# Performance work log

Hardware: AMD Instinct MI355X
Metric: run time of the kernel (lower is better)

Reference implementation:

```python
import jax, jax.numpy as jnp
import numpy as np
from jax import lax

PEAK_THRESH = 0.1
PAF_SCORE_THRESH = 0.05
PAF_COUNT_THRESH = 0.8
P = 30   # max peaks kept per joint (vectorized stand-in for data-dependent nonzero())
S = 10   # samples along each limb line (torch.linspace steps=10)

# standard COCO person skeleton: 19 limbs over 17 keypoints
SKELETON = np.array([
    [15, 13], [13, 11], [16, 14], [14, 12], [11, 12], [5, 11], [6, 12], [5, 6],
    [5, 7], [6, 8], [7, 9], [8, 10], [1, 2], [0, 1], [0, 2], [1, 3], [2, 4],
    [3, 5], [4, 6],
])  # (L=19, 2)


def setup_inputs() -> dict:
    key = jax.random.key(0)
    k1, k2 = jax.random.split(key)
    heat_pred = jax.random.uniform(k1, (32, 17, 160, 160), dtype=jnp.float32)
    paf_pred = jax.random.normal(k2, (32, 38, 160, 160), dtype=jnp.float32)
    return {"heat_pred": heat_pred, "paf_pred": paf_pred}


def _forward(heat_pred, paf_pred):
    B, K, H, W = heat_pred.shape
    L = SKELETON.shape[0]

    # ---- 3x3 peak NMS (max_pool2d k=3, s=1, p=1) ----
    pooled = lax.reduce_window(heat_pred, -jnp.inf, lax.max,
                               (1, 1, 3, 3), (1, 1, 1, 1), 'SAME')
    is_peak = (heat_pred == pooled) & (heat_pred > PEAK_THRESH)

    # ---- dense subpixel (1D Newton) offsets ----
    r = jnp.roll(heat_pred, -1, -1); l = jnp.roll(heat_pred, 1, -1)
    d = jnp.roll(heat_pred, -1, -2); u = jnp.roll(heat_pred, 1, -2)
    dx_raw = 0.5 * (r - l); dy_raw = 0.5 * (d - u)
    dxx = r + l - 2.0 * heat_pred; dyy = d + u - 2.0 * heat_pred
    safe_dxx = jnp.where(jnp.abs(dxx) > 1e-6, -dxx, 1.0)
    safe_dyy = jnp.where(jnp.abs(dyy) > 1e-6, -dyy, 1.0)
    dx = jnp.where(jnp.abs(dxx) > 1e-6, dx_raw / safe_dxx, dx_raw)
    dy = jnp.where(jnp.abs(dyy) > 1e-6, dy_raw / safe_dyy, dy_raw)
    xi = jnp.arange(W); yi = jnp.arange(H)
    interior = (((yi > 0) & (yi < H - 1))[:, None]
                & ((xi > 0) & (xi < W - 1))[None, :])
    dx = jnp.where(interior, dx, 0.0)
    dy = jnp.where(interior, dy, 0.0)

    # ---- top-P peaks per (batch, joint) ----
    NEG = jnp.float32(-1e9)
    flat = jnp.where(is_peak, heat_pred, NEG).reshape(B, K, H * W)
    scores, idx = lax.top_k(flat, P)                    # (B, K, P)
    valid = scores > PEAK_THRESH
    py = (idx // W).astype(jnp.float32)
    px = (idx % W).astype(jnp.float32)
    dxp = jnp.take_along_axis(dx.reshape(B, K, H * W), idx, axis=2)
    dyp = jnp.take_along_axis(dy.reshape(B, K, H * W), idx, axis=2)
    px = jnp.where(valid, px + dxp, 0.0)
    py = jnp.where(valid, py + dyp, 0.0)
    sc = jnp.where(valid, scores, 0.0)
    peaks = jnp.stack([px, py, sc], axis=-1)            # (B, K, P, 3)

    # ---- PAF line-integral connection scores for all candidate pairs ----
    a = SKELETON[:, 0]; b = SKELETON[:, 1]
    ax, ay, sa, va = px[:, a], py[:, a], sc[:, a], valid[:, a]   # (B, L, P)
    bx, by, sb, vb = px[:, b], py[:, b], sc[:, b], valid[:, b]
    dxl = bx[:, :, None, :] - ax[:, :, :, None]          # (B, L, P, P)
    dyl = by[:, :, None, :] - ay[:, :, :, None]
    norm = jnp.sqrt(dxl * dxl + dyl * dyl) + 1e-8
    vx = dxl / norm; vy = dyl / norm
    t = jnp.linspace(0.0, 1.0, S, dtype=jnp.float32)     # (S,)
    xs = ax[:, :, :, None, None] + t * dxl[..., None]    # (B, L, P, P, S)
    ys = ay[:, :, :, None, None] + t * dyl[..., None]
    ix = jnp.clip(jnp.round(xs), 0, W - 1).astype(jnp.int32)
    iy = jnp.clip(jnp.round(ys), 0, H - 1).astype(jnp.int32)
    lin = (iy * W + ix).reshape(B, L, P * P * S)
    paf = paf_pred.reshape(B, L, 2, H * W)
    vals_x = jnp.take_along_axis(paf[:, :, 0], lin, axis=2).reshape(B, L, P, P, S)
    vals_y = jnp.take_along_axis(paf[:, :, 1], lin, axis=2).reshape(B, L, P, P, S)
    vecs = vals_x * vx[..., None] + vals_y * vy[..., None]
    mean_score = vecs.mean(-1)                            # (B, L, P, P)
    valid_ratio = (vecs > PAF_SCORE_THRESH).astype(jnp.float32).mean(-1)
    pair_valid = va[:, :, :, None] & vb[:, :, None, :]
    cond = (mean_score > 0.0) & (valid_ratio > PAF_COUNT_THRESH) & pair_valid
    conn = jnp.where(cond,
                     mean_score + 0.5 * (sa[:, :, :, None] + sb[:, :, None, :]),
                     0.0)                                 # (B, L, P, P)
    return peaks, conn


def reference(heat_pred, paf_pred):
    return _forward(heat_pred, paf_pred)
```

## Files before the change

### kernel.cpp

```cpp
#include <hip/hip_runtime.h>
#include <cstdint>
#include <cstddef>
#include <cfloat>

static constexpr int BATCH = 32;
static constexpr int KJ    = 17;
static constexpr int LL    = 19;
static constexpr int HH    = 160;
static constexpr int WW    = 160;
static constexpr int PPK   = 30;
static constexpr int SS    = 10;
static constexpr int HW    = HH * WW;
static constexpr int CAP   = 4096;
static constexpr int CELLS = HW / 4;
static constexpr int CGW   = WW / 4;

__constant__ int d_ska[LL] = {15,13,16,14,11,5,6,5,5,6,7,8,1,0,0,1,2,3,4};
__constant__ int d_skb[LL] = {13,11,14,12,12,11,12,6,7,8,9,10,2,1,2,3,4,5,6};
__constant__ float d_ts[SS] = {
    0.0f,
    (float)(1.0/9.0), (float)(2.0/9.0), (float)(3.0/9.0),
    (float)(4.0/9.0), (float)(5.0/9.0), (float)(6.0/9.0),
    (float)(7.0/9.0), (float)(8.0/9.0),
    1.0f
};

__device__ __forceinline__ float max3f(float a, float b, float c) {
    return fmaxf(fmaxf(a, b), c);
}
__device__ __forceinline__ unsigned long long umax64(unsigned long long a, unsigned long long b) {
    return a > b ? a : b;
}

__global__ __launch_bounds__(256, 4) void peaks_kernel(const float* __restrict__ heat,
                                                       float* __restrict__ out)
{
    const int ch = blockIdx.x;
    const float* hp = heat + (size_t)ch * HW;

    __shared__ unsigned long long keys[CAP];
    __shared__ unsigned long long sel4[4 * PPK];
    __shared__ unsigned long long sel[PPK];
    __shared__ int cnt;

    const int tid  = threadIdx.x;
    const int lane = tid & 63;
    const int wave = tid >> 6;
    const unsigned long long ltmask = ((unsigned long long)1 << lane) - 1ull;

    if (tid == 0) cnt = 0;
    __syncthreads();

    for (int c = tid; c < CELLS; c += 256) {
        int y  = c / CGW;
        int cg = c - y * CGW;
        int x0 = cg * 4;
        int yu = (y > 0) ? y - 1 : 0;
        int yd = (y < HH - 1) ? y + 1 : HH - 1;

        const float* rc = hp + y  * WW + x0;
        const float* ru = hp + yu * WW + x0;
        const float* rd = hp + yd * WW + x0;

        float4 vc = *(const float4*)rc;
        float4 vu = *(const float4*)ru;
        float4 vd = *(const float4*)rd;
        bool hasL = (x0 > 0);
        bool hasR = (x0 + 4 < WW);
        float lc = hasL ? rc[-1] : -FLT_MAX;
        float lu = hasL ? ru[-1] : -FLT_MAX;
        float ld = hasL ? rd[-1] : -FLT_MAX;
        float rcx = hasR ? rc[4] : -FLT_MAX;
        float rux = hasR ? ru[4] : -FLT_MAX;
        float rdx = hasR ? rd[4] : -FLT_MAX;

        float mu0 = max3f(lu, vu.x, vu.y), mu1 = max3f(vu.x, vu.y, vu.z);
        float mu2 = max3f(vu.y, vu.z, vu.w), mu3 = max3f(vu.z, vu.w, rux);
        float mc0 = max3f(lc, vc.x, vc.y), mc1 = max3f(vc.x, vc.y, vc.z);
        float mc2 = max3f(vc.y, vc.z, vc.w), mc3 = max3f(vc.z, vc.w, rcx);
        float md0 = max3f(ld, vd.x, vd.y), md1 = max3f(vd.x, vd.y, vd.z);
        float md2 = max3f(vd.y, vd.z, vd.w), md3 = max3f(vd.z, vd.w, rdx);

        float nm0 = max3f(mu0, mc0, md0);
        float nm1 = max3f(mu1, mc1, md1);
        float nm2 = max3f(mu2, mc2, md2);
        float nm3 = max3f(mu3, mc3, md3);

        bool pk0 = (vc.x == nm0) && (vc.x > 0.1f);
        bool pk1 = (vc.y == nm1) && (vc.y > 0.1f);
        bool pk2 = (vc.z == nm2) && (vc.z > 0.1f);
        bool pk3 = (vc.w == nm3) && (vc.w > 0.1f);

        unsigned long long b0 = __ballot(pk0);
        unsigned long long b1 = __ballot(pk1);
        unsigned long long b2 = __ballot(pk2);
        unsigned long long b3 = __ballot(pk3);
        int c0 = __popcll(b0), c1 = __popcll(b1), c2 = __popcll(b2), c3 = __popcll(b3);
        int tot = c0 + c1 + c2 + c3;
        int base = 0;
        if (lane == 0 && tot > 0) base = atomicAdd(&cnt, tot);
        base = __shfl(base, 0);

        int idx0 = y * WW + x0;
        if (pk0) {
            int slot = base + __popcll(b0 & ltmask);
            if (slot < CAP)
                keys[slot] = ((unsigned long long)__float_as_uint(vc.x) << 32)
                           | (unsigned long long)(0xFFFFFFFFu - (unsigned)(idx0 + 0));
        }
        if (pk1) {
            int slot = base + c0 + __popcll(b1 & ltmask);
            if (slot < CAP)
                keys[slot] = ((unsigned long long)__float_as_uint(vc.y) << 32)
                           | (unsigned long long)(0xFFFFFFFFu - (unsigned)(idx0 + 1));
        }
        if (pk2) {
            int slot = base + c0 + c1 + __popcll(b2 & ltmask);
            if (slot < CAP)
                keys[slot] = ((unsigned long long)__float_as_uint(vc.z) << 32)
                           | (unsigned long long)(0xFFFFFFFFu - (unsigned)(idx0 + 2));
        }
        if (pk3) {
            int slot = base + c0 + c1 + c2 + __popcll(b3 & ltmask);
            if (slot < CAP)
                keys[slot] = ((unsigned long long)__float_as_uint(vc.w) << 32)
                           | (unsigned long long)(0xFFFFFFFFu - (unsigned)(idx0 + 3));
        }
    }
    __syncthreads();

    const int n = (cnt < CAP) ? cnt : CAP;

    unsigned long long k[16];
    {
        int base0 = wave * 1024 + lane;
        #pragma unroll
        for (int i = 0; i < 16; ++i) {
            int p = base0 + i * 64;
            k[i] = (p < n) ? keys[p] : 0ull;
        }
    }
    for (int r = 0; r < PPK; ++r) {
        unsigned long long best = k[0];
        #pragma unroll
        for (int i = 1; i < 16; ++i) best = umax64(best, k[i]);
        #pragma unroll
        for (int off = 1; off < 64; off <<= 1)
            best = umax64(best, (unsigned long long)__shfl_xor((long long)best, off));
        if (best != 0ull) {
            #pragma unroll
            for (int i = 0; i < 16; ++i)
                if (k[i] == best) k[i] = 0ull;
        }
        if (lane == 0) sel4[wave * PPK + r] = best;
    }
    __syncthreads();

    if (wave == 0) {
        unsigned long long m0 = sel4[lane];
        unsigned long long m1 = (lane + 64 < 4 * PPK) ? sel4[lane + 64] : 0ull;
        for (int r = 0; r < PPK; ++r) {
            unsigned long long best = umax64(m0, m1);
            #pragma unroll
            for (int off = 1; off < 64; off <<= 1)
                best = umax64(best, (unsigned long long)__shfl_xor((long long)best, off));
            if (best != 0ull) {
                if (m0 == best) m0 = 0ull;
                else if (m1 == best) m1 = 0ull;
            }
            if (lane == 0) sel[r] = best;
        }
    }
    __syncthreads();

    if (tid < PPK) {
        unsigned long long g = sel[tid];
        float px = 0.0f, py = 0.0f, sc = 0.0f;
        if (g != 0ull) {
            float v = __uint_as_float((unsigned int)(g >> 32));
            int idx = (int)(0xFFFFFFFFu - (unsigned int)(g & 0xFFFFFFFFull));
            int y = idx / WW;
            int x = idx - y * WW;
            float dx = 0.0f, dy = 0.0f;
            if (x > 0 && x < WW - 1 && y > 0 && y < HH - 1) {
                float r_ = hp[y * WW + x + 1];
                float l_ = hp[y * WW + x - 1];
                float dn = hp[(y + 1) * WW + x];
                float up = hp[(y - 1) * WW + x];
                float dx_raw = 0.5f * (r_ - l_);
                float dy_raw = 0.5f * (dn - up);
                float dxx = __fsub_rn(__fadd_rn(r_, l_), 2.0f * v);
                float dyy = __fsub_rn(__fadd_rn(dn, up), 2.0f * v);
                dx = (fabsf(dxx) > 1e-6f) ? (dx_raw / (-dxx)) : dx_raw;
                dy = (fabsf(dyy) > 1e-6f) ? (dy_raw / (-dyy)) : dy_raw;
            }
            px = __fadd_rn((float)x, dx);
            py = __fadd_rn((float)y, dy);
            sc = v;
        }
        float* o = out + ((size_t)ch * PPK + tid) * 3;
        o[0] = px;
        o[1] = py;
        o[2] = sc;
    }
}

__global__ __launch_bounds__(256) void conn_kernel(const float* __restrict__ paf,
                                                   const float* __restrict__ peaks,
                                                   float* __restrict__ conn)
{
    const int blk = blockIdx.x;
    const int bl  = blk >> 2;
    const int q   = blk & 3;
    const int b   = bl / LL;
    const int l   = bl - b * LL;

    const float* pafx = paf + (((size_t)b * (2 * LL)) + 2 * l) * HW;
    const float* pafy = pafx + HW;

    __shared__ float As[PPK * 3];
    __shared__ float Bs[PPK * 3];

    const int tid = threadIdx.x;
    {
        const float* pa = peaks + (((size_t)b * KJ) + d_ska[l]) * (PPK * 3);
        const float* pb = peaks + (((size_t)b * KJ) + d_skb[l]) * (PPK * 3);
        if (tid < PPK * 3)            As[tid] = pa[tid];
        else if (tid < 2 * PPK * 3)   Bs[tid - PPK * 3] = pb[tid - PPK * 3];
    }
    __syncthreads();

    const int p = q * 225 + tid;
    if (tid < 225 && p < PPK * PPK) {
        int i = p / PPK;
        int j = p - i * PPK;

        float ax = As[i * 3 + 0], ay = As[i * 3 + 1], sa = As[i * 3 + 2];
        float bx = Bs[j * 3 + 0], by = Bs[j * 3 + 1], sb = Bs[j * 3 + 2];
        bool va = sa > 0.1f;
        bool vb = sb > 0.1f;

        float dxl = __fsub_rn(bx, ax);
        float dyl = __fsub_rn(by, ay);
        float nsq = __fadd_rn(__fmul_rn(dxl, dxl), __fmul_rn(dyl, dyl));
        float nrm = __fadd_rn(sqrtf(nsq), 1e-8f);
        float vx  = dxl / nrm;
        float vy  = dyl / nrm;

        float vs[SS];
        int   cntc = 0;
        #pragma unroll
        for (int s = 0; s < SS; ++s) {
            float t  = d_ts[s];
            float xs = __fadd_rn(ax, __fmul_rn(t, dxl));
            float ys = __fadd_rn(ay, __fmul_rn(t, dyl));
            float rx = rintf(xs);
            float ry = rintf(ys);
            rx = fminf(fmaxf(rx, 0.0f), (float)(WW - 1));
            ry = fminf(fmaxf(ry, 0.0f), (float)(HH - 1));
            int ix = (int)rx;
            int iy = (int)ry;
            int lin = iy * WW + ix;
            float vxs = pafx[lin];
            float vys = pafy[lin];
            float vec = __fadd_rn(__fmul_rn(vxs, vx), __fmul_rn(vys, vy));
            vs[s] = vec;
            if (vec > 0.05f) ++cntc;
        }
        float s01 = __fadd_rn(vs[0], vs[1]);
        float s23 = __fadd_rn(vs[2], vs[3]);
        float s45 = __fadd_rn(vs[4], vs[5]);
        float s67 = __fadd_rn(vs[6], vs[7]);
        float sum = __fadd_rn(__fadd_rn(s01, s23), __fadd_rn(s45, s67));
        sum = __fadd_rn(sum, vs[8]);
        sum = __fadd_rn(sum, vs[9]);
        float mean = sum / 10.0f;

        bool cond = (mean > 0.0f) && (cntc >= 9) && va && vb;
        float val = 0.0f;
        if (cond) {
            val = __fadd_rn(mean, __fmul_rn(0.5f, __fadd_rn(sa, sb)));
        }
        conn[(size_t)bl * (PPK * PPK) + p] = val;
    }
}

extern "C" void kernel_launch(void* const* d_in, const int* in_sizes, int n_in,
                              void* d_out, int out_size, void* d_ws, size_t ws_size,
                              hipStream_t stream)
{
    const float* heat = (const float*)d_in[0];
    const float* paf  = (const float*)d_in[1];
    float* out = (float*)d_out;

    float* peaks_out = out;
    float* conn_out  = out + (size_t)BATCH * KJ * PPK * 3;

    hipLaunchKernelGGL(peaks_kernel, dim3(BATCH * KJ), dim3(256), 0, stream,
                       heat, peaks_out);
    hipLaunchKernelGGL(conn_kernel, dim3(BATCH * LL * 4), dim3(256), 0, stream,
                       paf, peaks_out, conn_out);
}
```

Before: 302.3 us.

## Split peak search into row strips with merge and stage PAF planes in LDS

Peak detection is split into four row-strip blocks per channel that each keep a local top-30, followed by a small merge kernel; a fused fallback is kept when workspace is too small. The connection kernel now processes one (batch, limb) per 512-thread block and streams PAF planes through shared memory in halves instead of gathering from global memory. This raises block-level parallelism for the peak scan and replaces scattered global loads with coalesced bulk loads, at the cost of an extra launch, more total PAF bytes read, and large LDS use limiting occupancy.

```diff
diff --git a/kernel.cpp b/kernel.cpp
--- a/kernel.cpp
+++ b/kernel.cpp
@@ -11,9 +11,15 @@
 static constexpr int PPK   = 30;
 static constexpr int SS    = 10;
 static constexpr int HW    = HH * WW;
-static constexpr int CAP   = 4096;
-static constexpr int CELLS = HW / 4;
 static constexpr int CGW   = WW / 4;
+
+static constexpr int NSTR  = 4;
+static constexpr int SROWS = HH / NSTR;
+static constexpr int SCAP  = 2048;
+static constexpr size_t WS_NEED = (size_t)BATCH * KJ * 128 * sizeof(unsigned long long);
+
+static constexpr int HROWS = 80;
+static constexpr int HCNT  = HROWS * WW;
 
 __constant__ int d_ska[LL] = {15,13,16,14,11,5,6,5,5,6,7,8,1,0,0,1,2,3,4};
 __constant__ int d_skb[LL] = {13,11,14,12,12,11,12,6,7,8,9,10,2,1,2,3,4,5,6};
@@ -32,15 +38,17 @@
     return a > b ? a : b;
 }
 
-__global__ __launch_bounds__(256, 4) void peaks_kernel(const float* __restrict__ heat,
-                                                       float* __restrict__ out)
+__global__ __launch_bounds__(256) void peaks_scan(const float* __restrict__ heat,
+                                                  unsigned long long* __restrict__ ws)
 {
-    const int ch = blockIdx.x;
+    const int blk   = blockIdx.x;
+    const int ch    = blk >> 2;
+    const int strip = blk & 3;
+    const int y0    = strip * SROWS;
     const float* hp = heat + (size_t)ch * HW;
 
-    __shared__ unsigned long long keys[CAP];
+    __shared__ unsigned long long keys[SCAP];
     __shared__ unsigned long long sel4[4 * PPK];
-    __shared__ unsigned long long sel[PPK];
     __shared__ int cnt;
 
     const int tid  = threadIdx.x;
@@ -51,9 +59,11 @@
     if (tid == 0) cnt = 0;
     __syncthreads();
 
-    for (int c = tid; c < CELLS; c += 256) {
-        int y  = c / CGW;
-        int cg = c - y * CGW;
+    const int cells = SROWS * CGW;
+    for (int c = tid; c < cells; c += 256) {
+        int ly = c / CGW;
+        int cg = c - ly * CGW;
+        int y  = y0 + ly;
         int x0 = cg * 4;
         int yu = (y > 0) ? y - 1 : 0;
         int yd = (y < HH - 1) ? y + 1 : HH - 1;
@@ -104,33 +114,211 @@
         int idx0 = y * WW + x0;
         if (pk0) {
             int slot = base + __popcll(b0 & ltmask);
-            if (slot < CAP)
+            if (slot < SCAP)
                 keys[slot] = ((unsigned long long)__float_as_uint(vc.x) << 32)
                            | (unsigned long long)(0xFFFFFFFFu - (unsigned)(idx0 + 0));
         }
         if (pk1) {
             int slot = base + c0 + __popcll(b1 & ltmask);
-            if (slot < CAP)
+            if (slot < SCAP)
                 keys[slot] = ((unsigned long long)__float_as_uint(vc.y) << 32)
                            | (unsigned long long)(0xFFFFFFFFu - (unsigned)(idx0 + 1));
         }
         if (pk2) {
             int slot = base + c0 + c1 + __popcll(b2 & ltmask);
-            if (slot < CAP)
+            if (slot < SCAP)
                 keys[slot] = ((unsigned long long)__float_as_uint(vc.z) << 32)
                            | (unsigned long long)(0xFFFFFFFFu - (unsigned)(idx0 + 2));
         }
         if (pk3) {
             int slot = base + c0 + c1 + c2 + __popcll(b3 & ltmask);
-            if (slot < CAP)
+            if (slot < SCAP)
                 keys[slot] = ((unsigned long long)__float_as_uint(vc.w) << 32)
                            | (unsigned long long)(0xFFFFFFFFu - (unsigned)(idx0 + 3));
         }
     }
     __syncthreads();
 
-    const int n = (cnt < CAP) ? cnt : CAP;
-
+    const int n = (cnt < SCAP) ? cnt : SCAP;
+
+    unsigned long long k[8];
+    {
+        int base0 = wave * 512 + lane;
+        #pragma unroll
+        for (int i = 0; i < 8; ++i) {
+            int p = base0 + i * 64;
+            k[i] = (p < n) ? keys[p] : 0ull;
+        }
+    }
+    for (int r = 0; r < PPK; ++r) {
+        unsigned long long best = k[0];
+        #pragma unroll
+        for (int i = 1; i < 8; ++i) best = umax64(best, k[i]);
+        #pragma unroll
+        for (int off = 1; off < 64; off <<= 1)
+            best = umax64(best, (unsigned long long)__shfl_xor((long long)best, off));
+        if (best != 0ull) {
+            #pragma unroll
+            for (int i = 0; i < 8; ++i)
+                if (k[i] == best) k[i] = 0ull;
+        }
+        if (lane == 0) sel4[wave * PPK + r] = best;
+    }
+    __syncthreads();
+
+    if (wave == 0) {
+        unsigned long long m0 = sel4[lane & 63 < 4 * PPK ? lane : 0];
+        m0 = (lane < 4 * PPK) ? sel4[lane] : 0ull;
+        unsigned long long m1 = (lane + 64 < 4 * PPK) ? sel4[lane + 64] : 0ull;
+        unsigned long long* wsout = ws + (size_t)ch * 128 + strip * PPK;
+        for (int r = 0; r < PPK; ++r) {
+            unsigned long long best = umax64(m0, m1);
+            #pragma unroll
+            for (int off = 1; off < 64; off <<= 1)
+                best = umax64(best, (unsigned long long)__shfl_xor((long long)best, off));
+            if (best != 0ull) {
+                if (m0 == best) m0 = 0ull;
+                else if (m1 == best) m1 = 0ull;
+            }
+            if (lane == 0) wsout[r] = best;
+        }
+    }
+}
+
+__global__ __launch_bounds__(64) void peaks_merge(const float* __restrict__ heat,
+                                                  const unsigned long long* __restrict__ ws,
+                                                  float* __restrict__ out)
+{
+    const int ch   = blockIdx.x;
+    const int lane = threadIdx.x;
+    const float* hp = heat + (size_t)ch * HW;
+    const unsigned long long* kp = ws + (size_t)ch * 128;
+
+    __shared__ unsigned long long sel[PPK];
+
+    unsigned long long m0 = (lane < 4 * PPK) ? kp[lane] : 0ull;
+    unsigned long long m1 = (lane + 64 < 4 * PPK) ? kp[lane + 64] : 0ull;
+    for (int r = 0; r < PPK; ++r) {
+        unsigned long long best = umax64(m0, m1);
+        #pragma unroll
+        for (int off = 1; off < 64; off <<= 1)
+            best = umax64(best, (unsigned long long)__shfl_xor((long long)best, off));
+        if (best != 0ull) {
+            if (m0 == best) m0 = 0ull;
+            else if (m1 == best) m1 = 0ull;
+        }
+        if (lane == 0) sel[r] = best;
+    }
+    __syncthreads();
+
+    if (lane < PPK) {
+        unsigned long long g = sel[lane];
+        float px = 0.0f, py = 0.0f, sc = 0.0f;
+        if (g != 0ull) {
+            float v = __uint_as_float((unsigned int)(g >> 32));
+            int idx = (int)(0xFFFFFFFFu - (unsigned int)(g & 0xFFFFFFFFull));
+            int y = idx / WW;
+            int x = idx - y * WW;
+            float dx = 0.0f, dy = 0.0f;
+            if (x > 0 && x < WW - 1 && y > 0 && y < HH - 1) {
+                float r_ = hp[y * WW + x + 1];
+                float l_ = hp[y * WW + x - 1];
+                float dn = hp[(y + 1) * WW + x];
+                float up = hp[(y - 1) * WW + x];
+                float dx_raw = 0.5f * (r_ - l_);
+                float dy_raw = 0.5f * (dn - up);
+                float dxx = __fsub_rn(__fadd_rn(r_, l_), 2.0f * v);
+                float dyy = __fsub_rn(__fadd_rn(dn, up), 2.0f * v);
+                dx = (fabsf(dxx) > 1e-6f) ? (dx_raw / (-dxx)) : dx_raw;
+                dy = (fabsf(dyy) > 1e-6f) ? (dy_raw / (-dyy)) : dy_raw;
+            }
+            px = __fadd_rn((float)x, dx);
+            py = __fadd_rn((float)y, dy);
+            sc = v;
+        }
+        float* o = out + ((size_t)ch * PPK + lane) * 3;
+        o[0] = px;
+        o[1] = py;
+        o[2] = sc;
+    }
+}
+
+static constexpr int FCAP = 4096;
+__global__ __launch_bounds__(256, 4) void peaks_fused(const float* __restrict__ heat,
+                                                      float* __restrict__ out)
+{
+    const int ch = blockIdx.x;
+    const float* hp = heat + (size_t)ch * HW;
+
+    __shared__ unsigned long long keys[FCAP];
+    __shared__ unsigned long long sel4[4 * PPK];
+    __shared__ unsigned long long sel[PPK];
+    __shared__ int cnt;
+
+    const int tid  = threadIdx.x;
+    const int lane = tid & 63;
+    const int wave = tid >> 6;
+    const unsigned long long ltmask = ((unsigned long long)1 << lane) - 1ull;
+
+    if (tid == 0) cnt = 0;
+    __syncthreads();
+
+    for (int c = tid; c < HW / 4; c += 256) {
+        int y  = c / CGW;
+        int cg = c - y * CGW;
+        int x0 = cg * 4;
+        int yu = (y > 0) ? y - 1 : 0;
+        int yd = (y < HH - 1) ? y + 1 : HH - 1;
+        const float* rc = hp + y  * WW + x0;
+        const float* ru = hp + yu * WW + x0;
+        const float* rd = hp + yd * WW + x0;
+        float4 vc = *(const float4*)rc;
+        float4 vu = *(const float4*)ru;
+        float4 vd = *(const float4*)rd;
+        bool hasL = (x0 > 0);
+        bool hasR = (x0 + 4 < WW);
+        float lc = hasL ? rc[-1] : -FLT_MAX;
+        float lu = hasL ? ru[-1] : -FLT_MAX;
+        float ld = hasL ? rd[-1] : -FLT_MAX;
+        float rcx = hasR ? rc[4] : -FLT_MAX;
+        float rux = hasR ? ru[4] : -FLT_MAX;
+        float rdx = hasR ? rd[4] : -FLT_MAX;
+        float mu0 = max3f(lu, vu.x, vu.y), mu1 = max3f(vu.x, vu.y, vu.z);
+        float mu2 = max3f(vu.y, vu.z, vu.w), mu3 = max3f(vu.z, vu.w, rux);
+        float mc0 = max3f(lc, vc.x, vc.y), mc1 = max3f(vc.x, vc.y, vc.z);
+        float mc2 = max3f(vc.y, vc.z, vc.w), mc3 = max3f(vc.z, vc.w, rcx);
+        float md0 = max3f(ld, vd.x, vd.y), md1 = max3f(vd.x, vd.y, vd.z);
+        float md2 = max3f(vd.y, vd.z, vd.w), md3 = max3f(vd.z, vd.w, rdx);
+        float nm0 = max3f(mu0, mc0, md0);
+        float nm1 = max3f(mu1, mc1, md1);
+        float nm2 = max3f(mu2, mc2, md2);
+        float nm3 = max3f(mu3, mc3, md3);
+        bool pk0 = (vc.x == nm0) && (vc.x > 0.1f);
+        bool pk1 = (vc.y == nm1) && (vc.y > 0.1f);
+        bool pk2 = (vc.z == nm2) && (vc.z > 0.1f);
+        bool pk3 = (vc.w == nm3) && (vc.w > 0.1f);
+        unsigned long long b0 = __ballot(pk0);
+        unsigned long long b1 = __ballot(pk1);
+        unsigned long long b2 = __ballot(pk2);
+        unsigned long long b3 = __ballot(pk3);
+        int c0 = __popcll(b0), c1 = __popcll(b1), c2 = __popcll(b2), c3 = __popcll(b3);
+        int tot = c0 + c1 + c2 + c3;
+        int base = 0;
+        if (lane == 0 && tot > 0) base = atomicAdd(&cnt, tot);
+        base = __shfl(base, 0);
+        int idx0 = y * WW + x0;
+        if (pk0) { int s = base + __popcll(b0 & ltmask); if (s < FCAP)
+            keys[s] = ((unsigned long long)__float_as_uint(vc.x) << 32) | (unsigned long long)(0xFFFFFFFFu - (unsigned)(idx0 + 0)); }
+        if (pk1) { int s = base + c0 + __popcll(b1 & ltmask); if (s < FCAP)
+            keys[s] = ((unsigned long long)__float_as_uint(vc.y) << 32) | (unsigned long long)(0xFFFFFFFFu - (unsigned)(idx0 + 1)); }
+        if (pk2) { int s = base + c0 + c1 + __popcll(b2 & ltmask); if (s < FCAP)
+            keys[s] = ((unsigned long long)__float_as_uint(vc.z) << 32) | (unsigned long long)(0xFFFFFFFFu - (unsigned)(idx0 + 2)); }
+        if (pk3) { int s = base + c0 + c1 + c2 + __popcll(b3 & ltmask); if (s < FCAP)
+            keys[s] = ((unsigned long long)__float_as_uint(vc.w) << 32) | (unsigned long long)(0xFFFFFFFFu - (unsigned)(idx0 + 3)); }
+    }
+    __syncthreads();
+
+    const int n = (cnt < FCAP) ? cnt : FCAP;
     unsigned long long k[16];
     {
         int base0 = wave * 1024 + lane;
@@ -155,9 +343,8 @@
         if (lane == 0) sel4[wave * PPK + r] = best;
     }
     __syncthreads();
-
     if (wave == 0) {
-        unsigned long long m0 = sel4[lane];
+        unsigned long long m0 = (lane < 4 * PPK) ? sel4[lane] : 0ull;
         unsigned long long m1 = (lane + 64 < 4 * PPK) ? sel4[lane + 64] : 0ull;
         for (int r = 0; r < PPK; ++r) {
             unsigned long long best = umax64(m0, m1);
@@ -172,7 +359,6 @@
         }
     }
     __syncthreads();
-
     if (tid < PPK) {
         unsigned long long g = sel[tid];
         float px = 0.0f, py = 0.0f, sc = 0.0f;
@@ -205,21 +391,18 @@
     }
 }
 
-__global__ __launch_bounds__(256) void conn_kernel(const float* __restrict__ paf,
-                                                   const float* __restrict__ peaks,
-                                                   float* __restrict__ conn)
+__global__ __launch_bounds__(512, 2) void conn_kernel(const float* __restrict__ paf,
+                                                      const float* __restrict__ peaks,
+                                                      float* __restrict__ conn)
 {
-    const int blk = blockIdx.x;
-    const int bl  = blk >> 2;
-    const int q   = blk & 3;
-    const int b   = bl / LL;
-    const int l   = bl - b * LL;
-
-    const float* pafx = paf + (((size_t)b * (2 * LL)) + 2 * l) * HW;
-    const float* pafy = pafx + HW;
-
+    const int bl = blockIdx.x;
+    const int b  = bl / LL;
+    const int l  = bl - b * LL;
+
+    __shared__ float4 plane4[HCNT / 4];
     __shared__ float As[PPK * 3];
     __shared__ float Bs[PPK * 3];
+    float* plane = (float*)plane4;
 
     const int tid = threadIdx.x;
     {
@@ -230,25 +413,25 @@
     }
     __syncthreads();
 
-    const int p = q * 225 + tid;
-    if (tid < 225 && p < PPK * PPK) {
+    const int npair = (tid + 512 < PPK * PPK) ? 2 : 1;
+    int   lin[2][SS];
+    float acc[2][SS];
+    float vxp[2], vyp[2], sap[2], sbp[2];
+
+    for (int q = 0; q < npair; ++q) {
+        int p = tid + q * 512;
         int i = p / PPK;
         int j = p - i * PPK;
-
         float ax = As[i * 3 + 0], ay = As[i * 3 + 1], sa = As[i * 3 + 2];
         float bx = Bs[j * 3 + 0], by = Bs[j * 3 + 1], sb = Bs[j * 3 + 2];
-        bool va = sa > 0.1f;
-        bool vb = sb > 0.1f;
-
         float dxl = __fsub_rn(bx, ax);
         float dyl = __fsub_rn(by, ay);
         float nsq = __fadd_rn(__fmul_rn(dxl, dxl), __fmul_rn(dyl, dyl));
         float nrm = __fadd_rn(sqrtf(nsq), 1e-8f);
-        float vx  = dxl / nrm;
-        float vy  = dyl / nrm;
-
-        float vs[SS];
-        int   cntc = 0;
+        vxp[q] = dxl / nrm;
+        vyp[q] = dyl / nrm;
+        sap[q] = sa;
+        sbp[q] = sb;
         #pragma unroll
         for (int s = 0; s < SS; ++s) {
             float t  = d_ts[s];
@@ -258,29 +441,53 @@
             float ry = rintf(ys);
             rx = fminf(fmaxf(rx, 0.0f), (float)(WW - 1));
             ry = fminf(fmaxf(ry, 0.0f), (float)(HH - 1));
-            int ix = (int)rx;
-            int iy = (int)ry;
-            int lin = iy * WW + ix;
-            float vxs = pafx[lin];
-            float vys = pafy[lin];
-            float vec = __fadd_rn(__fmul_rn(vxs, vx), __fmul_rn(vys, vy));
-            vs[s] = vec;
-            if (vec > 0.05f) ++cntc;
-        }
-        float s01 = __fadd_rn(vs[0], vs[1]);
-        float s23 = __fadd_rn(vs[2], vs[3]);
-        float s45 = __fadd_rn(vs[4], vs[5]);
-        float s67 = __fadd_rn(vs[6], vs[7]);
+            lin[q][s] = (int)ry * WW + (int)rx;
+        }
+    }
+
+    for (int phase = 0; phase < 4; ++phase) {
+        const int comp = phase >> 1;
+        const int half = phase & 1;
+        const float4* src = (const float4*)(paf + (((size_t)b * (2 * LL)) + 2 * l + comp) * HW
+                                                + half * HCNT);
+        __syncthreads();
+        for (int i = tid; i < HCNT / 4; i += 512)
+            plane4[i] = src[i];
+        __syncthreads();
+
+        const int lo = half * HCNT;
+        for (int q = 0; q < npair; ++q) {
+            #pragma unroll
+            for (int s = 0; s < SS; ++s) {
+                int lrel = lin[q][s] - lo;
+                if ((unsigned)lrel < (unsigned)HCNT) {
+                    float v = plane[lrel];
+                    if (comp == 0) acc[q][s] = __fmul_rn(v, vxp[q]);
+                    else           acc[q][s] = __fadd_rn(acc[q][s], __fmul_rn(v, vyp[q]));
+                }
+            }
+        }
+    }
+
+    for (int q = 0; q < npair; ++q) {
+        int p = tid + q * 512;
+        int cntc = 0;
+        #pragma unroll
+        for (int s = 0; s < SS; ++s)
+            if (acc[q][s] > 0.05f) ++cntc;
+        float s01 = __fadd_rn(acc[q][0], acc[q][1]);
+        float s23 = __fadd_rn(acc[q][2], acc[q][3]);
+        float s45 = __fadd_rn(acc[q][4], acc[q][5]);
+        float s67 = __fadd_rn(acc[q][6], acc[q][7]);
         float sum = __fadd_rn(__fadd_rn(s01, s23), __fadd_rn(s45, s67));
-        sum = __fadd_rn(sum, vs[8]);
-        sum = __fadd_rn(sum, vs[9]);
+        sum = __fadd_rn(sum, acc[q][8]);
+        sum = __fadd_rn(sum, acc[q][9]);
         float mean = sum / 10.0f;
-
+        bool va = sap[q] > 0.1f;
+        bool vb = sbp[q] > 0.1f;
         bool cond = (mean > 0.0f) && (cntc >= 9) && va && vb;
         float val = 0.0f;
-        if (cond) {
-            val = __fadd_rn(mean, __fmul_rn(0.5f, __fadd_rn(sa, sb)));
-        }
+        if (cond) val = __fadd_rn(mean, __fmul_rn(0.5f, __fadd_rn(sap[q], sbp[q])));
         conn[(size_t)bl * (PPK * PPK) + p] = val;
     }
 }
@@ -296,8 +503,16 @@
     float* peaks_out = out;
     float* conn_out  = out + (size_t)BATCH * KJ * PPK * 3;
 
-    hipLaunchKernelGGL(peaks_kernel, dim3(BATCH * KJ), dim3(256), 0, stream,
-                       heat, peaks_out);
-    hipLaunchKernelGGL(conn_kernel, dim3(BATCH * LL * 4), dim3(256), 0, stream,
+    if (ws_size >= WS_NEED) {
+        unsigned long long* ws64 = (unsigned long long*)d_ws;
+        hipLaunchKernelGGL(peaks_scan, dim3(BATCH * KJ * NSTR), dim3(256), 0, stream,
+                           heat, ws64);
+        hipLaunchKernelGGL(peaks_merge, dim3(BATCH * KJ), dim3(64), 0, stream,
+                           heat, ws64, peaks_out);
+    } else {
+        hipLaunchKernelGGL(peaks_fused, dim3(BATCH * KJ), dim3(256), 0, stream,
+                           heat, peaks_out);
+    }
+    hipLaunchKernelGGL(conn_kernel, dim3(BATCH * LL), dim3(512), 0, stream,
                        paf, peaks_out, conn_out);
 }
```

Measured after the change: 320.2 us. +5.9%, slower.

## Stream full PAF planes through double-buffered LDS in conn kernel; widen peaks blocks

Applied to the files above, without the earlier changes.

The connection kernel now uses one 512-thread block per (batch, limb). It streams both PAF planes through shared memory in 40-row double-buffered chunks and gathers samples from LDS instead of doing scattered global loads. This turns random gathers into fully coalesced streaming reads, but it now reads every PAF pixel even though only a few thousand samples are needed, and it uses large LDS per block. The peaks kernel also moves to 512 threads with 8 waves per partial top-k.

```diff
diff --git a/kernel.cpp b/kernel.cpp
--- a/kernel.cpp
+++ b/kernel.cpp
@@ -11,9 +11,12 @@
 static constexpr int PPK   = 30;
 static constexpr int SS    = 10;
 static constexpr int HW    = HH * WW;
+static constexpr int CGW   = WW / 4;
 static constexpr int CAP   = 4096;
-static constexpr int CELLS = HW / 4;
-static constexpr int CGW   = WW / 4;
+
+static constexpr int QROWS = 40;
+static constexpr int QCNT  = QROWS * WW;
+static constexpr int QF4   = QCNT / 4;
 
 __constant__ int d_ska[LL] = {15,13,16,14,11,5,6,5,5,6,7,8,1,0,0,1,2,3,4};
 __constant__ int d_skb[LL] = {13,11,14,12,12,11,12,6,7,8,9,10,2,1,2,3,4,5,6};
@@ -32,14 +35,14 @@
     return a > b ? a : b;
 }
 
-__global__ __launch_bounds__(256, 4) void peaks_kernel(const float* __restrict__ heat,
+__global__ __launch_bounds__(512, 4) void peaks_kernel(const float* __restrict__ heat,
                                                        float* __restrict__ out)
 {
     const int ch = blockIdx.x;
     const float* hp = heat + (size_t)ch * HW;
 
     __shared__ unsigned long long keys[CAP];
-    __shared__ unsigned long long sel4[4 * PPK];
+    __shared__ unsigned long long sel8[8 * PPK];
     __shared__ unsigned long long sel[PPK];
     __shared__ int cnt;
 
@@ -51,7 +54,7 @@
     if (tid == 0) cnt = 0;
     __syncthreads();
 
-    for (int c = tid; c < CELLS; c += 256) {
+    for (int c = tid; c < HW / 4; c += 512) {
         int y  = c / CGW;
         int cg = c - y * CGW;
         int x0 = cg * 4;
@@ -102,40 +105,24 @@
         base = __shfl(base, 0);
 
         int idx0 = y * WW + x0;
-        if (pk0) {
-            int slot = base + __popcll(b0 & ltmask);
-            if (slot < CAP)
-                keys[slot] = ((unsigned long long)__float_as_uint(vc.x) << 32)
-                           | (unsigned long long)(0xFFFFFFFFu - (unsigned)(idx0 + 0));
-        }
-        if (pk1) {
-            int slot = base + c0 + __popcll(b1 & ltmask);
-            if (slot < CAP)
-                keys[slot] = ((unsigned long long)__float_as_uint(vc.y) << 32)
-                           | (unsigned long long)(0xFFFFFFFFu - (unsigned)(idx0 + 1));
-        }
-        if (pk2) {
-            int slot = base + c0 + c1 + __popcll(b2 & ltmask);
-            if (slot < CAP)
-                keys[slot] = ((unsigned long long)__float_as_uint(vc.z) << 32)
-                           | (unsigned long long)(0xFFFFFFFFu - (unsigned)(idx0 + 2));
-        }
-        if (pk3) {
-            int slot = base + c0 + c1 + c2 + __popcll(b3 & ltmask);
-            if (slot < CAP)
-                keys[slot] = ((unsigned long long)__float_as_uint(vc.w) << 32)
-                           | (unsigned long long)(0xFFFFFFFFu - (unsigned)(idx0 + 3));
-        }
+        if (pk0) { int s = base + __popcll(b0 & ltmask); if (s < CAP)
+            keys[s] = ((unsigned long long)__float_as_uint(vc.x) << 32) | (unsigned long long)(0xFFFFFFFFu - (unsigned)(idx0 + 0)); }
+        if (pk1) { int s = base + c0 + __popcll(b1 & ltmask); if (s < CAP)
+            keys[s] = ((unsigned long long)__float_as_uint(vc.y) << 32) | (unsigned long long)(0xFFFFFFFFu - (unsigned)(idx0 + 1)); }
+        if (pk2) { int s = base + c0 + c1 + __popcll(b2 & ltmask); if (s < CAP)
+            keys[s] = ((unsigned long long)__float_as_uint(vc.z) << 32) | (unsigned long long)(0xFFFFFFFFu - (unsigned)(idx0 + 2)); }
+        if (pk3) { int s = base + c0 + c1 + c2 + __popcll(b3 & ltmask); if (s < CAP)
+            keys[s] = ((unsigned long long)__float_as_uint(vc.w) << 32) | (unsigned long long)(0xFFFFFFFFu - (unsigned)(idx0 + 3)); }
     }
     __syncthreads();
 
     const int n = (cnt < CAP) ? cnt : CAP;
 
-    unsigned long long k[16];
+    unsigned long long k[8];
     {
-        int base0 = wave * 1024 + lane;
-        #pragma unroll
-        for (int i = 0; i < 16; ++i) {
+        int base0 = wave * 512 + lane;
+        #pragma unroll
+        for (int i = 0; i < 8; ++i) {
             int p = base0 + i * 64;
             k[i] = (p < n) ? keys[p] : 0ull;
         }
@@ -143,30 +130,35 @@
     for (int r = 0; r < PPK; ++r) {
         unsigned long long best = k[0];
         #pragma unroll
-        for (int i = 1; i < 16; ++i) best = umax64(best, k[i]);
+        for (int i = 1; i < 8; ++i) best = umax64(best, k[i]);
         #pragma unroll
         for (int off = 1; off < 64; off <<= 1)
             best = umax64(best, (unsigned long long)__shfl_xor((long long)best, off));
         if (best != 0ull) {
             #pragma unroll
-            for (int i = 0; i < 16; ++i)
+            for (int i = 0; i < 8; ++i)
                 if (k[i] == best) k[i] = 0ull;
         }
-        if (lane == 0) sel4[wave * PPK + r] = best;
+        if (lane == 0) sel8[wave * PPK + r] = best;
     }
     __syncthreads();
 
     if (wave == 0) {
-        unsigned long long m0 = sel4[lane];
-        unsigned long long m1 = (lane + 64 < 4 * PPK) ? sel4[lane + 64] : 0ull;
+        unsigned long long m[4];
+        #pragma unroll
+        for (int i = 0; i < 4; ++i) {
+            int p = lane + i * 64;
+            m[i] = (p < 8 * PPK) ? sel8[p] : 0ull;
+        }
         for (int r = 0; r < PPK; ++r) {
-            unsigned long long best = umax64(m0, m1);
+            unsigned long long best = umax64(umax64(m[0], m[1]), umax64(m[2], m[3]));
             #pragma unroll
             for (int off = 1; off < 64; off <<= 1)
                 best = umax64(best, (unsigned long long)__shfl_xor((long long)best, off));
             if (best != 0ull) {
-                if (m0 == best) m0 = 0ull;
-                else if (m1 == best) m1 = 0ull;
+                #pragma unroll
+                for (int i = 0; i < 4; ++i)
+                    if (m[i] == best) m[i] = 0ull;
             }
             if (lane == 0) sel[r] = best;
         }
@@ -205,19 +197,15 @@
     }
 }
 
-__global__ __launch_bounds__(256) void conn_kernel(const float* __restrict__ paf,
-                                                   const float* __restrict__ peaks,
-                                                   float* __restrict__ conn)
+__global__ __launch_bounds__(512, 6) void conn_kernel(const float* __restrict__ paf,
+                                                      const float* __restrict__ peaks,
+                                                      float* __restrict__ conn)
 {
-    const int blk = blockIdx.x;
-    const int bl  = blk >> 2;
-    const int q   = blk & 3;
-    const int b   = bl / LL;
-    const int l   = bl - b * LL;
-
-    const float* pafx = paf + (((size_t)b * (2 * LL)) + 2 * l) * HW;
-    const float* pafy = pafx + HW;
-
+    const int bl = blockIdx.x;
+    const int b  = bl / LL;
+    const int l  = bl - b * LL;
+
+    __shared__ float buf[2][QCNT];
     __shared__ float As[PPK * 3];
     __shared__ float Bs[PPK * 3];
 
@@ -230,25 +218,25 @@
     }
     __syncthreads();
 
-    const int p = q * 225 + tid;
-    if (tid < 225 && p < PPK * PPK) {
+    const int npair = (tid + 512 < PPK * PPK) ? 2 : ((tid < PPK * PPK) ? 1 : 0);
+    int   lin[2][SS];
+    float accv[2][SS];
+    float vxp[2], vyp[2], sap[2], sbp[2];
+
+    for (int q = 0; q < npair; ++q) {
+        int p = tid + q * 512;
         int i = p / PPK;
         int j = p - i * PPK;
-
         float ax = As[i * 3 + 0], ay = As[i * 3 + 1], sa = As[i * 3 + 2];
         float bx = Bs[j * 3 + 0], by = Bs[j * 3 + 1], sb = Bs[j * 3 + 2];
-        bool va = sa > 0.1f;
-        bool vb = sb > 0.1f;
-
         float dxl = __fsub_rn(bx, ax);
         float dyl = __fsub_rn(by, ay);
         float nsq = __fadd_rn(__fmul_rn(dxl, dxl), __fmul_rn(dyl, dyl));
         float nrm = __fadd_rn(sqrtf(nsq), 1e-8f);
-        float vx  = dxl / nrm;
-        float vy  = dyl / nrm;
-
-        float vs[SS];
-        int   cntc = 0;
+        vxp[q] = dxl / nrm;
+        vyp[q] = dyl / nrm;
+        sap[q] = sa;
+        sbp[q] = sb;
         #pragma unroll
         for (int s = 0; s < SS; ++s) {
             float t  = d_ts[s];
@@ -258,29 +246,82 @@
             float ry = rintf(ys);
             rx = fminf(fmaxf(rx, 0.0f), (float)(WW - 1));
             ry = fminf(fmaxf(ry, 0.0f), (float)(HH - 1));
-            int ix = (int)rx;
-            int iy = (int)ry;
-            int lin = iy * WW + ix;
-            float vxs = pafx[lin];
-            float vys = pafy[lin];
-            float vec = __fadd_rn(__fmul_rn(vxs, vx), __fmul_rn(vys, vy));
-            vs[s] = vec;
-            if (vec > 0.05f) ++cntc;
-        }
-        float s01 = __fadd_rn(vs[0], vs[1]);
-        float s23 = __fadd_rn(vs[2], vs[3]);
-        float s45 = __fadd_rn(vs[4], vs[5]);
-        float s67 = __fadd_rn(vs[6], vs[7]);
+            lin[q][s] = (int)ry * WW + (int)rx;
+        }
+    }
+
+    const float* src = paf + (((size_t)b * (2 * LL)) + 2 * l) * HW;
+
+    float4 r0, r1, r2, r3;
+    {
+        const float4* s4 = (const float4*)src;
+        r0 = s4[tid];
+        r1 = s4[tid + 512];
+        r2 = s4[tid + 1024];
+        if (tid < QF4 - 1536) r3 = s4[tid + 1536];
+        float4* b4 = (float4*)buf[0];
+        b4[tid] = r0;
+        b4[tid + 512] = r1;
+        b4[tid + 1024] = r2;
+        if (tid < QF4 - 1536) b4[tid + 1536] = r3;
+    }
+    __syncthreads();
+
+    for (int qq = 0; qq < 8; ++qq) {
+        const int cur = qq & 1;
+        if (qq < 7) {
+            const int nq = qq + 1;
+            const float4* s4 = (const float4*)(src + (size_t)(nq >> 2) * HW + (nq & 3) * QCNT);
+            r0 = s4[tid];
+            r1 = s4[tid + 512];
+            r2 = s4[tid + 1024];
+            if (tid < QF4 - 1536) r3 = s4[tid + 1536];
+        }
+        {
+            const int comp = qq >> 2;
+            const int lo   = (qq & 3) * QCNT;
+            for (int q = 0; q < npair; ++q) {
+                #pragma unroll
+                for (int s = 0; s < SS; ++s) {
+                    int lrel = lin[q][s] - lo;
+                    if ((unsigned)lrel < (unsigned)QCNT) {
+                        float v = buf[cur][lrel];
+                        if (comp == 0) accv[q][s] = __fmul_rn(v, vxp[q]);
+                        else           accv[q][s] = __fadd_rn(accv[q][s], __fmul_rn(v, vyp[q]));
+                    }
+                }
+            }
+        }
+        __syncthreads();
+        if (qq < 7) {
+            float4* b4 = (float4*)buf[1 - cur];
+            b4[tid] = r0;
+            b4[tid + 512] = r1;
+            b4[tid + 1024] = r2;
+            if (tid < QF4 - 1536) b4[tid + 1536] = r3;
+            __syncthreads();
+        }
+    }
+
+    for (int q = 0; q < npair; ++q) {
+        int p = tid + q * 512;
+        int cntc = 0;
+        #pragma unroll
+        for (int s = 0; s < SS; ++s)
+            if (accv[q][s] > 0.05f) ++cntc;
+        float s01 = __fadd_rn(accv[q][0], accv[q][1]);
+        float s23 = __fadd_rn(accv[q][2], accv[q][3]);
+        float s45 = __fadd_rn(accv[q][4], accv[q][5]);
+        float s67 = __fadd_rn(accv[q][6], accv[q][7]);
         float sum = __fadd_rn(__fadd_rn(s01, s23), __fadd_rn(s45, s67));
-        sum = __fadd_rn(sum, vs[8]);
-        sum = __fadd_rn(sum, vs[9]);
+        sum = __fadd_rn(sum, accv[q][8]);
+        sum = __fadd_rn(sum, accv[q][9]);
         float mean = sum / 10.0f;
-
+        bool va = sap[q] > 0.1f;
+        bool vb = sbp[q] > 0.1f;
         bool cond = (mean > 0.0f) && (cntc >= 9) && va && vb;
         float val = 0.0f;
-        if (cond) {
-            val = __fadd_rn(mean, __fmul_rn(0.5f, __fadd_rn(sa, sb)));
-        }
+        if (cond) val = __fadd_rn(mean, __fmul_rn(0.5f, __fadd_rn(sap[q], sbp[q])));
         conn[(size_t)bl * (PPK * PPK) + p] = val;
     }
 }
@@ -296,8 +337,8 @@
     float* peaks_out = out;
     float* conn_out  = out + (size_t)BATCH * KJ * PPK * 3;
 
-    hipLaunchKernelGGL(peaks_kernel, dim3(BATCH * KJ), dim3(256), 0, stream,
+    hipLaunchKernelGGL(peaks_kernel, dim3(BATCH * KJ), dim3(512), 0, stream,
                        heat, peaks_out);
-    hipLaunchKernelGGL(conn_kernel, dim3(BATCH * LL * 4), dim3(256), 0, stream,
+    hipLaunchKernelGGL(conn_kernel, dim3(BATCH * LL), dim3(512), 0, stream,
                        paf, peaks_out, conn_out);
 }
```

Result: slower. 384.8 us (+27.3%).
